# Kernel optimization log

Hardware: AMD Instinct MI355X
Metric: run time of the kernel (lower is better)

The kernel has to match this reference:

```python
import jax, jax.numpy as jnp
import numpy as np

B, E, I, H, O = 8192, 8, 512, 1024, 512


def setup_inputs() -> dict:
    key = jax.random.key(0)
    ks = jax.random.split(key, 8)
    # Xavier-uniform-ish scales for expert weights
    s1 = float(np.sqrt(6.0 / (I + H)))
    s2 = float(np.sqrt(6.0 / (H + H)))
    s3 = float(np.sqrt(6.0 / (H + O)))
    return {
        "X": jax.random.normal(ks[0], (B, I), dtype=jnp.float32),
        "W": jax.random.uniform(ks[1], (B, E), dtype=jnp.float32),
        "W1": jax.random.uniform(ks[2], (E, H, I), minval=-s1, maxval=s1, dtype=jnp.float32),
        "b1": jnp.zeros((E, H), dtype=jnp.float32),
        "W2": jax.random.uniform(ks[3], (E, H, H), minval=-s2, maxval=s2, dtype=jnp.float32),
        "b2": jnp.zeros((E, H), dtype=jnp.float32),
        "W3": jax.random.uniform(ks[4], (E, O, H), minval=-s3, maxval=s3, dtype=jnp.float32),
        "b3": jnp.zeros((E, O), dtype=jnp.float32),
    }


def reference(X, W, W1, b1, W2, b2, W3, b3):
    # NOTE: original torch code calls F.softmax(W, dim=1) but discards the
    # result; raw W is used as the per-expert mixing weight. We match that.
    # Layer 1: per-expert linear [B,E,H], then gate-weighted sum over E.
    pre1 = jnp.einsum('bi,ehi->beh', X, W1) + b1          # [B,E,H]
    mid1 = jax.nn.elu(jnp.einsum('be,beh->bh', W, pre1))  # [B,H]
    pre2 = jnp.einsum('bh,egh->beg', mid1, W2) + b2       # [B,E,H]
    mid2 = jax.nn.elu(jnp.einsum('be,beh->bh', W, pre2))  # [B,H]
    pre3 = jnp.einsum('bh,eoh->beo', mid2, W3) + b3       # [B,E,O]
    out = jnp.einsum('be,beo->bo', W, pre3)               # [B,O]
    return out
```

## Files before the change

kernel.cpp:

```cpp
#include <hip/hip_runtime.h>
#include <hip/hip_bf16.h>
#include <cstdint>
#include <cstddef>

typedef __attribute__((ext_vector_type(8))) short bf16x8;
typedef __attribute__((ext_vector_type(8))) unsigned short u16x8;
typedef __attribute__((ext_vector_type(4))) float f32x4;
typedef unsigned short u16;

__device__ __forceinline__ u16 f2bf(float f) {
    unsigned int u = __float_as_uint(f);
    u += 0x7fffu + ((u >> 16) & 1u);
    return (u16)(u >> 16);
}
__device__ __forceinline__ float bf2f(u16 u) {
    return __uint_as_float(((unsigned int)u) << 16);
}

__device__ __forceinline__ void gload16(const void* g, void* l) {
    __builtin_amdgcn_global_load_lds((const __attribute__((address_space(1))) void*)g,
                                     (__attribute__((address_space(3))) void*)l,
                                     16, 0, 0);
}

__global__ void cvt_f32_bf16(const float* __restrict__ in, u16* __restrict__ out, int n4) {
    int i = blockIdx.x * blockDim.x + threadIdx.x;
    if (i < n4) {
        float4 v = ((const float4*)in)[i];
        ushort4 o;
        o.x = f2bf(v.x); o.y = f2bf(v.y); o.z = f2bf(v.z); o.w = f2bf(v.w);
        ((ushort4*)out)[i] = o;
    }
}

__global__ void make_atilde_f32(const float* __restrict__ A, const float* __restrict__ gate,
                                u16* __restrict__ out, int log2K) {
    const size_t idx = ((size_t)blockIdx.x * 256 + threadIdx.x) * 8;
    const int K = 1 << log2K;
    const size_t b = idx >> (log2K + 3);
    const int rem = (int)(idx - (b << (log2K + 3)));
    const int e = rem >> log2K;
    const int k = rem & (K - 1);
    const float g = gate[b * 8 + e];
    const float* src = A + b * (size_t)K + k;
    float4 v0 = ((const float4*)src)[0];
    float4 v1 = ((const float4*)src)[1];
    u16x8 r;
    r[0] = f2bf(g * v0.x); r[1] = f2bf(g * v0.y); r[2] = f2bf(g * v0.z); r[3] = f2bf(g * v0.w);
    r[4] = f2bf(g * v1.x); r[5] = f2bf(g * v1.y); r[6] = f2bf(g * v1.z); r[7] = f2bf(g * v1.w);
    *(u16x8*)(out + idx) = r;
}

__global__ void make_atilde_bf16(const u16* __restrict__ A, const float* __restrict__ gate,
                                 u16* __restrict__ out, int log2K) {
    const size_t idx = ((size_t)blockIdx.x * 256 + threadIdx.x) * 8;
    const int K = 1 << log2K;
    const size_t b = idx >> (log2K + 3);
    const int rem = (int)(idx - (b << (log2K + 3)));
    const int e = rem >> log2K;
    const int k = rem & (K - 1);
    const float g = gate[b * 8 + e];
    u16x8 a = *(const u16x8*)(A + b * (size_t)K + k);
    u16x8 r;
    #pragma unroll
    for (int j = 0; j < 8; ++j) r[j] = f2bf(g * bf2f(a[j]));
    *(u16x8*)(out + idx) = r;
}

__global__ __launch_bounds__(512, 2)
void moe_gemm_8p(const u16* __restrict__ At, const u16* __restrict__ Bw,
                 float* __restrict__ P,
                 int N, int K, int Ktot, int log2nk, int kts, int bxbits) {
    __shared__ char lds[2][65536];

    const int tid  = threadIdx.x;
    const int lane = tid & 63;
    const int wave = tid >> 6;
    const int wm   = wave >> 2;
    const int wn   = wave & 3;
    const int fr   = lane & 15;
    const int fg   = lane >> 4;
    const int swz  = (fr & 7) << 4;

    const int bid  = blockIdx.x;
    const int wgid = (bid & 7) * 32 + (bid >> 3);
    const int bx   = wgid & ((1 << bxbits) - 1);
    const int by   = (wgid >> bxbits) & 31;
    const int s    = wgid >> (bxbits + 5);
    const int m0   = by * 256;
    const int n0   = bx * 256;

    int rowA[2], rowB[2], ldso[2];
    #pragma unroll
    for (int it = 0; it < 2; ++it) {
        const int o  = (it * 8 + wave) * 1024 + lane * 16;
        const int r  = o >> 7;
        const int cb = (o & 127) ^ ((r & 7) << 4);
        rowA[it] = r * (Ktot * 2) + cb;
        rowB[it] = r * (K * 2) + cb;
        ldso[it] = o;
    }

    const char* Ab0 = (const char*)(At + (size_t)m0 * Ktot);
    const char* Ab1 = Ab0 + (size_t)128 * Ktot * 2;
    const char* Bb0 = (const char*)(Bw + (size_t)n0 * K);
    const char* Bb1 = Bb0 + (size_t)128 * K * 2;
    const size_t Best = (size_t)N * K * 2;
    const int nkm = (1 << log2nk) - 1;
    const int kt0 = s * kts;

#define STAGE_A(BUF, KTG) do { \
    const char* _a0 = Ab0 + (size_t)(KTG) * 128; \
    const char* _a1 = Ab1 + (size_t)(KTG) * 128; \
    char* _l = lds[BUF]; \
    gload16(_a0 + rowA[0], _l + ldso[0]); \
    gload16(_a0 + rowA[1], _l + ldso[1]); \
    gload16(_a1 + rowA[0], _l + 16384 + ldso[0]); \
    gload16(_a1 + rowA[1], _l + 16384 + ldso[1]); \
} while (0)

#define STAGE_B(BUF, KTG) do { \
    const int _kg = (KTG); \
    const size_t _bo = (size_t)(_kg >> log2nk) * Best + (size_t)(_kg & nkm) * 128; \
    char* _l = lds[BUF] + 32768; \
    gload16(Bb0 + _bo + rowB[0], _l + ldso[0]); \
    gload16(Bb0 + _bo + rowB[1], _l + ldso[1]); \
    gload16(Bb1 + _bo + rowB[0], _l + 16384 + ldso[0]); \
    gload16(Bb1 + _bo + rowB[1], _l + 16384 + ldso[1]); \
} while (0)

#define PH_BAR() do { \
    __builtin_amdgcn_sched_barrier(0); \
    __builtin_amdgcn_s_barrier(); \
    __builtin_amdgcn_sched_barrier(0); \
} while (0)

    f32x4 acc[8][4];
    #pragma unroll
    for (int i = 0; i < 8; ++i)
        #pragma unroll
        for (int j = 0; j < 4; ++j) acc[i][j] = f32x4{0.f, 0.f, 0.f, 0.f};

    bf16x8 af[2][4], bfA[2][2], bfB[2][2];

    STAGE_A(0, kt0);
    STAGE_B(0, kt0);
    STAGE_A(1, kt0 + 1);
    __builtin_amdgcn_sched_barrier(0);
    asm volatile("s_waitcnt vmcnt(4)" ::: "memory");
    __builtin_amdgcn_s_barrier();
    __builtin_amdgcn_sched_barrier(0);

#define FRAME(BUF, TREL) do { \
    const int _tr = (TREL); \
    const char* _abase = lds[BUF] + wm * 16384 + fr * 128; \
    const char* _bbase = lds[BUF] + 32768 + (wn >> 1) * 16384 + ((wn & 1) * 64 + fr) * 128; \
    const int _k0 = (fg * 16) ^ swz; \
    const int _k1 = (64 + fg * 16) ^ swz; \
     \
    _Pragma("unroll") for (int i = 0; i < 4; ++i) { \
        af[0][i] = *(const bf16x8*)(_abase + i * 2048 + _k0); \
        af[1][i] = *(const bf16x8*)(_abase + i * 2048 + _k1); } \
    _Pragma("unroll") for (int j = 0; j < 2; ++j) { \
        bfA[0][j] = *(const bf16x8*)(_bbase + j * 2048 + _k0); \
        bfA[1][j] = *(const bf16x8*)(_bbase + j * 2048 + _k1); } \
    if (_tr + 1 < kts) STAGE_B((BUF) ^ 1, kt0 + _tr + 1); \
    PH_BAR(); \
    __builtin_amdgcn_s_setprio(1); \
    _Pragma("unroll") for (int i = 0; i < 4; ++i) \
    _Pragma("unroll") for (int j = 0; j < 2; ++j) { \
        acc[i][j] = __builtin_amdgcn_mfma_f32_16x16x32_bf16(af[0][i], bfA[0][j], acc[i][j], 0, 0, 0); \
        acc[i][j] = __builtin_amdgcn_mfma_f32_16x16x32_bf16(af[1][i], bfA[1][j], acc[i][j], 0, 0, 0); } \
    __builtin_amdgcn_s_setprio(0); \
    PH_BAR(); \
     \
    _Pragma("unroll") for (int j = 0; j < 2; ++j) { \
        bfB[0][j] = *(const bf16x8*)(_bbase + (2 + j) * 2048 + _k0); \
        bfB[1][j] = *(const bf16x8*)(_bbase + (2 + j) * 2048 + _k1); } \
    PH_BAR(); \
    __builtin_amdgcn_s_setprio(1); \
    _Pragma("unroll") for (int i = 0; i < 4; ++i) \
    _Pragma("unroll") for (int j = 0; j < 2; ++j) { \
        acc[i][2 + j] = __builtin_amdgcn_mfma_f32_16x16x32_bf16(af[0][i], bfB[0][j], acc[i][2 + j], 0, 0, 0); \
        acc[i][2 + j] = __builtin_amdgcn_mfma_f32_16x16x32_bf16(af[1][i], bfB[1][j], acc[i][2 + j], 0, 0, 0); } \
    __builtin_amdgcn_s_setprio(0); \
    PH_BAR(); \
     \
    _Pragma("unroll") for (int i = 0; i < 4; ++i) { \
        af[0][i] = *(const bf16x8*)(_abase + (4 + i) * 2048 + _k0); \
        af[1][i] = *(const bf16x8*)(_abase + (4 + i) * 2048 + _k1); } \
    PH_BAR(); \
    __builtin_amdgcn_s_setprio(1); \
    _Pragma("unroll") for (int i = 0; i < 4; ++i) \
    _Pragma("unroll") for (int j = 0; j < 2; ++j) { \
        acc[4 + i][2 + j] = __builtin_amdgcn_mfma_f32_16x16x32_bf16(af[0][i], bfB[0][j], acc[4 + i][2 + j], 0, 0, 0); \
        acc[4 + i][2 + j] = __builtin_amdgcn_mfma_f32_16x16x32_bf16(af[1][i], bfB[1][j], acc[4 + i][2 + j], 0, 0, 0); } \
    __builtin_amdgcn_s_setprio(0); \
    PH_BAR(); \
     \
    if (_tr + 2 < kts) { \
        STAGE_A(BUF, kt0 + _tr + 2); \
        __builtin_amdgcn_sched_barrier(0); \
        asm volatile("s_waitcnt vmcnt(4)" ::: "memory"); \
    } else { \
        __builtin_amdgcn_sched_barrier(0); \
        asm volatile("s_waitcnt vmcnt(0)" ::: "memory"); \
    } \
    __builtin_amdgcn_s_barrier(); \
    __builtin_amdgcn_sched_barrier(0); \
    __builtin_amdgcn_s_setprio(1); \
    _Pragma("unroll") for (int i = 0; i < 4; ++i) \
    _Pragma("unroll") for (int j = 0; j < 2; ++j) { \
        acc[4 + i][j] = __builtin_amdgcn_mfma_f32_16x16x32_bf16(af[0][i], bfA[0][j], acc[4 + i][j], 0, 0, 0); \
        acc[4 + i][j] = __builtin_amdgcn_mfma_f32_16x16x32_bf16(af[1][i], bfA[1][j], acc[4 + i][j], 0, 0, 0); } \
    __builtin_amdgcn_s_setprio(0); \
    PH_BAR(); \
} while (0)

    for (int t = 0; t < kts; t += 2) {
        FRAME(0, t);
        FRAME(1, t + 1);
    }

    float* Pb = P + ((size_t)s * 8192 + m0 + wm * 128) * N + (n0 + wn * 64);
    #pragma unroll
    for (int mi = 0; mi < 8; ++mi)
        #pragma unroll
        for (int j = 0; j < 4; ++j) {
            const int r = mi * 16 + fg * 4 + j;
            #pragma unroll
            for (int ni = 0; ni < 4; ++ni)
                Pb[(size_t)r * N + ni * 16 + fr] = acc[mi][ni][j];
        }
#undef FRAME
#undef PH_BAR
#undef STAGE_A
#undef STAGE_B
}

template<int S, bool ELU_ACT, bool OUT_BF16>
__global__ void moe_reduce(const float* __restrict__ P,
                           const float* __restrict__ gate,
                           const float* __restrict__ bias,
                           void* __restrict__ outp,
                           int log2N, int n4total) {
    const int stride = gridDim.x * blockDim.x;
    const size_t MN = ((size_t)n4total) * 4;
    for (int i = blockIdx.x * blockDim.x + threadIdx.x; i < n4total; i += stride) {
        const size_t el = (size_t)i * 4;
        const size_t b = el >> log2N;
        const int n = (int)(el & ((1 << log2N) - 1));
        float4 v = ((const float4*)P)[i];
        #pragma unroll
        for (int s = 1; s < S; ++s) {
            float4 p = *(const float4*)(P + (size_t)s * MN + el);
            v.x += p.x; v.y += p.y; v.z += p.z; v.w += p.w;
        }
        #pragma unroll
        for (int e = 0; e < 8; ++e) {
            const float g = gate[b * 8 + e];
            float4 bb = *(const float4*)(bias + ((size_t)e << log2N) + n);
            v.x += g * bb.x; v.y += g * bb.y; v.z += g * bb.z; v.w += g * bb.w;
        }
        if (ELU_ACT) {
            v.x = v.x > 0.f ? v.x : expm1f(v.x);
            v.y = v.y > 0.f ? v.y : expm1f(v.y);
            v.z = v.z > 0.f ? v.z : expm1f(v.z);
            v.w = v.w > 0.f ? v.w : expm1f(v.w);
        }
        if (OUT_BF16) {
            ushort4 o; o.x = f2bf(v.x); o.y = f2bf(v.y); o.z = f2bf(v.z); o.w = f2bf(v.w);
            ((ushort4*)outp)[i] = o;
        } else {
            ((float4*)outp)[i] = v;
        }
    }
}

extern "C" void kernel_launch(void* const* d_in, const int* in_sizes, int n_in,
                              void* d_out, int out_size, void* d_ws, size_t ws_size,
                              hipStream_t stream) {
    const float* X  = (const float*)d_in[0];
    const float* W  = (const float*)d_in[1];
    const float* W1 = (const float*)d_in[2];
    const float* b1 = (const float*)d_in[3];
    const float* W2 = (const float*)d_in[4];
    const float* b2 = (const float*)d_in[5];
    const float* W3 = (const float*)d_in[6];
    const float* b3 = (const float*)d_in[7];
    float* out = (float*)d_out;

    char* ws = (char*)d_ws;
    u16* W1b  = (u16*)ws;  ws += (size_t)8 * 1024 * 512 * 2;
    u16* W2b  = (u16*)ws;  ws += (size_t)8 * 1024 * 1024 * 2;
    u16* W3b  = (u16*)ws;  ws += (size_t)8 * 512 * 1024 * 2;
    u16* mid1 = (u16*)ws;  ws += (size_t)8192 * 1024 * 2;
    u16* mid2 = (u16*)ws;  ws += (size_t)8192 * 1024 * 2;
    u16* At1  = (u16*)ws;  ws += (size_t)8192 * 4096 * 2;
    u16* At2  = (u16*)ws;  ws += (size_t)8192 * 8192 * 2;

    float* P1 = (float*)At2;
    float* P2 = (float*)At1;
    float* P3 = (float*)At1;

    cvt_f32_bf16<<<4096, 256, 0, stream>>>(W1, W1b, 4194304 / 4);
    cvt_f32_bf16<<<8192, 256, 0, stream>>>(W2, W2b, 8388608 / 4);
    cvt_f32_bf16<<<4096, 256, 0, stream>>>(W3, W3b, 4194304 / 4);

    dim3 blk(256);

    make_atilde_f32<<<16384, blk, 0, stream>>>(X, W, At1, 9);
    moe_gemm_8p<<<256, 512, 0, stream>>>(At1, W1b, P1, 1024, 512, 4096, 3, 32, 2);
    moe_reduce<2, true, true><<<2048, blk, 0, stream>>>(P1, W, b1, (void*)mid1, 10, 8192 * 1024 / 4);

    make_atilde_bf16<<<32768, blk, 0, stream>>>(mid1, W, At2, 10);
    moe_gemm_8p<<<256, 512, 0, stream>>>(At2, W2b, P2, 1024, 1024, 8192, 4, 64, 2);
    moe_reduce<2, true, true><<<2048, blk, 0, stream>>>(P2, W, b2, (void*)mid2, 10, 8192 * 1024 / 4);

    make_atilde_bf16<<<32768, blk, 0, stream>>>(mid2, W, At2, 10);
    moe_gemm_8p<<<256, 512, 0, stream>>>(At2, W3b, P3, 512, 1024, 8192, 4, 32, 1);
    moe_reduce<4, false, false><<<2048, blk, 0, stream>>>(P3, W, b3, (void*)out, 9, 8192 * 512 / 4);
}
```

Measured before the change: 402.1 us.

## Cut GEMM K-loop barriers to two per tile and fuse reduce with gate-scaling

The GEMM main loop goes from eight workgroup barriers per K tile to two. The B stage for the next tile is issued up front, and the A restage is placed between the last two MFMA groups. Separately, the layer-2 split-K reduce, bias, ELU and the gate-scaled bf16 A-tilde construction are fused into one kernel, removing the mid2 round trip and one launch. With fewer barriers, waves drift further apart and lose the phase interleaving the old scheme enforced.

```diff
diff --git a/kernel.cpp b/kernel.cpp
--- a/kernel.cpp
+++ b/kernel.cpp
@@ -68,7 +68,7 @@
 }
 
 __global__ __launch_bounds__(512, 2)
-void moe_gemm_8p(const u16* __restrict__ At, const u16* __restrict__ Bw,
+void moe_gemm_2b(const u16* __restrict__ At, const u16* __restrict__ Bw,
                  float* __restrict__ P,
                  int N, int K, int Ktot, int log2nk, int kts, int bxbits) {
     __shared__ char lds[2][65536];
@@ -129,12 +129,6 @@
     gload16(Bb1 + _bo + rowB[1], _l + 16384 + ldso[1]); \
 } while (0)
 
-#define PH_BAR() do { \
-    __builtin_amdgcn_sched_barrier(0); \
-    __builtin_amdgcn_s_barrier(); \
-    __builtin_amdgcn_sched_barrier(0); \
-} while (0)
-
     f32x4 acc[8][4];
     #pragma unroll
     for (int i = 0; i < 8; ++i)
@@ -151,75 +145,89 @@
     __builtin_amdgcn_s_barrier();
     __builtin_amdgcn_sched_barrier(0);
 
-#define FRAME(BUF, TREL) do { \
-    const int _tr = (TREL); \
-    const char* _abase = lds[BUF] + wm * 16384 + fr * 128; \
-    const char* _bbase = lds[BUF] + 32768 + (wn >> 1) * 16384 + ((wn & 1) * 64 + fr) * 128; \
-    const int _k0 = (fg * 16) ^ swz; \
-    const int _k1 = (64 + fg * 16) ^ swz; \
-     \
-    _Pragma("unroll") for (int i = 0; i < 4; ++i) { \
-        af[0][i] = *(const bf16x8*)(_abase + i * 2048 + _k0); \
-        af[1][i] = *(const bf16x8*)(_abase + i * 2048 + _k1); } \
-    _Pragma("unroll") for (int j = 0; j < 2; ++j) { \
-        bfA[0][j] = *(const bf16x8*)(_bbase + j * 2048 + _k0); \
-        bfA[1][j] = *(const bf16x8*)(_bbase + j * 2048 + _k1); } \
-    if (_tr + 1 < kts) STAGE_B((BUF) ^ 1, kt0 + _tr + 1); \
-    PH_BAR(); \
-    __builtin_amdgcn_s_setprio(1); \
-    _Pragma("unroll") for (int i = 0; i < 4; ++i) \
-    _Pragma("unroll") for (int j = 0; j < 2; ++j) { \
-        acc[i][j] = __builtin_amdgcn_mfma_f32_16x16x32_bf16(af[0][i], bfA[0][j], acc[i][j], 0, 0, 0); \
-        acc[i][j] = __builtin_amdgcn_mfma_f32_16x16x32_bf16(af[1][i], bfA[1][j], acc[i][j], 0, 0, 0); } \
-    __builtin_amdgcn_s_setprio(0); \
-    PH_BAR(); \
-     \
-    _Pragma("unroll") for (int j = 0; j < 2; ++j) { \
-        bfB[0][j] = *(const bf16x8*)(_bbase + (2 + j) * 2048 + _k0); \
-        bfB[1][j] = *(const bf16x8*)(_bbase + (2 + j) * 2048 + _k1); } \
-    PH_BAR(); \
-    __builtin_amdgcn_s_setprio(1); \
-    _Pragma("unroll") for (int i = 0; i < 4; ++i) \
-    _Pragma("unroll") for (int j = 0; j < 2; ++j) { \
-        acc[i][2 + j] = __builtin_amdgcn_mfma_f32_16x16x32_bf16(af[0][i], bfB[0][j], acc[i][2 + j], 0, 0, 0); \
-        acc[i][2 + j] = __builtin_amdgcn_mfma_f32_16x16x32_bf16(af[1][i], bfB[1][j], acc[i][2 + j], 0, 0, 0); } \
-    __builtin_amdgcn_s_setprio(0); \
-    PH_BAR(); \
-     \
-    _Pragma("unroll") for (int i = 0; i < 4; ++i) { \
-        af[0][i] = *(const bf16x8*)(_abase + (4 + i) * 2048 + _k0); \
-        af[1][i] = *(const bf16x8*)(_abase + (4 + i) * 2048 + _k1); } \
-    PH_BAR(); \
-    __builtin_amdgcn_s_setprio(1); \
-    _Pragma("unroll") for (int i = 0; i < 4; ++i) \
-    _Pragma("unroll") for (int j = 0; j < 2; ++j) { \
-        acc[4 + i][2 + j] = __builtin_amdgcn_mfma_f32_16x16x32_bf16(af[0][i], bfB[0][j], acc[4 + i][2 + j], 0, 0, 0); \
-        acc[4 + i][2 + j] = __builtin_amdgcn_mfma_f32_16x16x32_bf16(af[1][i], bfB[1][j], acc[4 + i][2 + j], 0, 0, 0); } \
-    __builtin_amdgcn_s_setprio(0); \
-    PH_BAR(); \
-     \
-    if (_tr + 2 < kts) { \
-        STAGE_A(BUF, kt0 + _tr + 2); \
-        __builtin_amdgcn_sched_barrier(0); \
-        asm volatile("s_waitcnt vmcnt(4)" ::: "memory"); \
-    } else { \
-        __builtin_amdgcn_sched_barrier(0); \
-        asm volatile("s_waitcnt vmcnt(0)" ::: "memory"); \
-    } \
-    __builtin_amdgcn_s_barrier(); \
-    __builtin_amdgcn_sched_barrier(0); \
-    __builtin_amdgcn_s_setprio(1); \
-    _Pragma("unroll") for (int i = 0; i < 4; ++i) \
-    _Pragma("unroll") for (int j = 0; j < 2; ++j) { \
-        acc[4 + i][j] = __builtin_amdgcn_mfma_f32_16x16x32_bf16(af[0][i], bfA[0][j], acc[4 + i][j], 0, 0, 0); \
-        acc[4 + i][j] = __builtin_amdgcn_mfma_f32_16x16x32_bf16(af[1][i], bfA[1][j], acc[4 + i][j], 0, 0, 0); } \
-    __builtin_amdgcn_s_setprio(0); \
-    PH_BAR(); \
-} while (0)
-
-    for (int t = 0; t < kts; t += 2) {
-        FRAME(0, t);
-        FRAME(1, t + 1);
+    for (int t = 0; t < kts; ++t) {
+        const int BUF = t & 1;
+        const char* _abase = lds[BUF] + wm * 16384 + fr * 128;
+        const char* _bbase = lds[BUF] + 32768 + (wn >> 1) * 16384 + ((wn & 1) * 64 + fr) * 128;
+        const int k0 = (fg * 16) ^ swz;
+        const int k1 = (64 + fg * 16) ^ swz;
+
+        if (t + 1 < kts) STAGE_B(BUF ^ 1, kt0 + t + 1);
+
+        #pragma unroll
+        for (int i = 0; i < 4; ++i) {
+            af[0][i] = *(const bf16x8*)(_abase + i * 2048 + k0);
+            af[1][i] = *(const bf16x8*)(_abase + i * 2048 + k1);
+        }
+        #pragma unroll
+        for (int j = 0; j < 2; ++j) {
+            bfA[0][j] = *(const bf16x8*)(_bbase + j * 2048 + k0);
+            bfA[1][j] = *(const bf16x8*)(_bbase + j * 2048 + k1);
+        }
+        __builtin_amdgcn_s_setprio(1);
+        #pragma unroll
+        for (int i = 0; i < 4; ++i)
+            #pragma unroll
+            for (int j = 0; j < 2; ++j) {
+                acc[i][j] = __builtin_amdgcn_mfma_f32_16x16x32_bf16(af[0][i], bfA[0][j], acc[i][j], 0, 0, 0);
+                acc[i][j] = __builtin_amdgcn_mfma_f32_16x16x32_bf16(af[1][i], bfA[1][j], acc[i][j], 0, 0, 0);
+            }
+        __builtin_amdgcn_s_setprio(0);
+
+        #pragma unroll
+        for (int j = 0; j < 2; ++j) {
+            bfB[0][j] = *(const bf16x8*)(_bbase + (2 + j) * 2048 + k0);
+            bfB[1][j] = *(const bf16x8*)(_bbase + (2 + j) * 2048 + k1);
+        }
+        __builtin_amdgcn_s_setprio(1);
+        #pragma unroll
+        for (int i = 0; i < 4; ++i)
+            #pragma unroll
+            for (int j = 0; j < 2; ++j) {
+                acc[i][2 + j] = __builtin_amdgcn_mfma_f32_16x16x32_bf16(af[0][i], bfB[0][j], acc[i][2 + j], 0, 0, 0);
+                acc[i][2 + j] = __builtin_amdgcn_mfma_f32_16x16x32_bf16(af[1][i], bfB[1][j], acc[i][2 + j], 0, 0, 0);
+            }
+        __builtin_amdgcn_s_setprio(0);
+
+        #pragma unroll
+        for (int i = 0; i < 4; ++i) {
+            af[0][i] = *(const bf16x8*)(_abase + (4 + i) * 2048 + k0);
+            af[1][i] = *(const bf16x8*)(_abase + (4 + i) * 2048 + k1);
+        }
+        __builtin_amdgcn_s_setprio(1);
+        #pragma unroll
+        for (int i = 0; i < 4; ++i)
+            #pragma unroll
+            for (int j = 0; j < 2; ++j) {
+                acc[4 + i][2 + j] = __builtin_amdgcn_mfma_f32_16x16x32_bf16(af[0][i], bfB[0][j], acc[4 + i][2 + j], 0, 0, 0);
+                acc[4 + i][2 + j] = __builtin_amdgcn_mfma_f32_16x16x32_bf16(af[1][i], bfB[1][j], acc[4 + i][2 + j], 0, 0, 0);
+            }
+        __builtin_amdgcn_s_setprio(0);
+
+        __builtin_amdgcn_sched_barrier(0);
+        __builtin_amdgcn_s_barrier();
+        __builtin_amdgcn_sched_barrier(0);
+
+        if (t + 2 < kts) STAGE_A(BUF, kt0 + t + 2);
+
+        __builtin_amdgcn_s_setprio(1);
+        #pragma unroll
+        for (int i = 0; i < 4; ++i)
+            #pragma unroll
+            for (int j = 0; j < 2; ++j) {
+                acc[4 + i][j] = __builtin_amdgcn_mfma_f32_16x16x32_bf16(af[0][i], bfA[0][j], acc[4 + i][j], 0, 0, 0);
+                acc[4 + i][j] = __builtin_amdgcn_mfma_f32_16x16x32_bf16(af[1][i], bfA[1][j], acc[4 + i][j], 0, 0, 0);
+            }
+        __builtin_amdgcn_s_setprio(0);
+
+        __builtin_amdgcn_sched_barrier(0);
+        if (t + 2 < kts) {
+            asm volatile("s_waitcnt vmcnt(4)" ::: "memory");
+        } else {
+            asm volatile("s_waitcnt vmcnt(0)" ::: "memory");
+        }
+        __builtin_amdgcn_s_barrier();
+        __builtin_amdgcn_sched_barrier(0);
     }
 
     float* Pb = P + ((size_t)s * 8192 + m0 + wm * 128) * N + (n0 + wn * 64);
@@ -232,8 +240,6 @@
             for (int ni = 0; ni < 4; ++ni)
                 Pb[(size_t)r * N + ni * 16 + fr] = acc[mi][ni][j];
         }
-#undef FRAME
-#undef PH_BAR
 #undef STAGE_A
 #undef STAGE_B
 }
@@ -277,6 +283,46 @@
     }
 }
 
+__global__ void reduce_atilde2(const float* __restrict__ P,
+                               const float* __restrict__ gate,
+                               const float* __restrict__ bias,
+                               u16* __restrict__ At) {
+    const int idx = blockIdx.x * 256 + threadIdx.x;
+    const int h = (idx & 127) * 8;
+    const size_t b = idx >> 7;
+    const size_t MH = (size_t)8192 * 1024;
+    const float* p = P + b * 1024 + h;
+    float4 v0 = ((const float4*)p)[0];
+    float4 v1 = ((const float4*)p)[1];
+    {
+        const float* p1 = p + MH;
+        float4 a0 = ((const float4*)p1)[0], a1 = ((const float4*)p1)[1];
+        v0.x += a0.x; v0.y += a0.y; v0.z += a0.z; v0.w += a0.w;
+        v1.x += a1.x; v1.y += a1.y; v1.z += a1.z; v1.w += a1.w;
+    }
+    float4 g0 = *(const float4*)&gate[b * 8];
+    float4 g1 = *(const float4*)&gate[b * 8 + 4];
+    float gg[8] = {g0.x, g0.y, g0.z, g0.w, g1.x, g1.y, g1.z, g1.w};
+    #pragma unroll
+    for (int e = 0; e < 8; ++e) {
+        const float* bb = bias + e * 1024 + h;
+        float4 b0 = ((const float4*)bb)[0], b1 = ((const float4*)bb)[1];
+        v0.x += gg[e] * b0.x; v0.y += gg[e] * b0.y; v0.z += gg[e] * b0.z; v0.w += gg[e] * b0.w;
+        v1.x += gg[e] * b1.x; v1.y += gg[e] * b1.y; v1.z += gg[e] * b1.z; v1.w += gg[e] * b1.w;
+    }
+    float m[8] = {v0.x, v0.y, v0.z, v0.w, v1.x, v1.y, v1.z, v1.w};
+    #pragma unroll
+    for (int j = 0; j < 8; ++j) m[j] = m[j] > 0.f ? m[j] : expm1f(m[j]);
+    u16* o = At + b * 8192 + h;
+    #pragma unroll
+    for (int e = 0; e < 8; ++e) {
+        u16x8 r;
+        #pragma unroll
+        for (int j = 0; j < 8; ++j) r[j] = f2bf(gg[e] * m[j]);
+        *(u16x8*)(o + e * 1024) = r;
+    }
+}
+
 extern "C" void kernel_launch(void* const* d_in, const int* in_sizes, int n_in,
                               void* d_out, int out_size, void* d_ws, size_t ws_size,
                               hipStream_t stream) {
@@ -298,6 +344,7 @@
     u16* mid2 = (u16*)ws;  ws += (size_t)8192 * 1024 * 2;
     u16* At1  = (u16*)ws;  ws += (size_t)8192 * 4096 * 2;
     u16* At2  = (u16*)ws;  ws += (size_t)8192 * 8192 * 2;
+    (void)mid2;
 
     float* P1 = (float*)At2;
     float* P2 = (float*)At1;
@@ -310,14 +357,13 @@
     dim3 blk(256);
 
     make_atilde_f32<<<16384, blk, 0, stream>>>(X, W, At1, 9);
-    moe_gemm_8p<<<256, 512, 0, stream>>>(At1, W1b, P1, 1024, 512, 4096, 3, 32, 2);
+    moe_gemm_2b<<<256, 512, 0, stream>>>(At1, W1b, P1, 1024, 512, 4096, 3, 32, 2);
     moe_reduce<2, true, true><<<2048, blk, 0, stream>>>(P1, W, b1, (void*)mid1, 10, 8192 * 1024 / 4);
 
     make_atilde_bf16<<<32768, blk, 0, stream>>>(mid1, W, At2, 10);
-    moe_gemm_8p<<<256, 512, 0, stream>>>(At2, W2b, P2, 1024, 1024, 8192, 4, 64, 2);
-    moe_reduce<2, true, true><<<2048, blk, 0, stream>>>(P2, W, b2, (void*)mid2, 10, 8192 * 1024 / 4);
-
-    make_atilde_bf16<<<32768, blk, 0, stream>>>(mid2, W, At2, 10);
-    moe_gemm_8p<<<256, 512, 0, stream>>>(At2, W3b, P3, 512, 1024, 8192, 4, 32, 1);
+    moe_gemm_2b<<<256, 512, 0, stream>>>(At2, W2b, P2, 1024, 1024, 8192, 4, 64, 2);
+    reduce_atilde2<<<4096, blk, 0, stream>>>(P2, W, b2, At2);
+
+    moe_gemm_2b<<<256, 512, 0, stream>>>(At2, W3b, P3, 512, 1024, 8192, 4, 32, 1);
     moe_reduce<4, false, false><<<2048, blk, 0, stream>>>(P3, W, b3, (void*)out, 9, 8192 * 512 / 4);
 }
```

Result: faster. 378.4 us (-5.9%).

## Restructure GEMM pipeline to one barrier per k-tile and fuse reduce with atilde

Applied to the files above, without the earlier changes.

The GEMM main loop drops the phased schedule, which had many barriers per tile and an A-tile prefetch two stages ahead. It now issues the next A and B tiles into the other buffer at the start of each k-tile and synchronizes once at the end with a full vmcnt(0) wait. Separately, the layer-2 split-K reduction, bias, ELU and gate-scaled bf16 A-tilde construction are fused into one kernel, removing the mid2 round trip and a launch. The simpler pipeline reduces barrier overhead but exposes global-load latency more, since it waits for all loads at every tile.

```diff
diff --git a/kernel.cpp b/kernel.cpp
--- a/kernel.cpp
+++ b/kernel.cpp
@@ -68,7 +68,7 @@
 }
 
 __global__ __launch_bounds__(512, 2)
-void moe_gemm_8p(const u16* __restrict__ At, const u16* __restrict__ Bw,
+void moe_gemm_1b(const u16* __restrict__ At, const u16* __restrict__ Bw,
                  float* __restrict__ P,
                  int N, int K, int Ktot, int log2nk, int kts, int bxbits) {
     __shared__ char lds[2][65536];
@@ -129,97 +129,77 @@
     gload16(Bb1 + _bo + rowB[1], _l + 16384 + ldso[1]); \
 } while (0)
 
-#define PH_BAR() do { \
+    f32x4 acc[8][4];
+    #pragma unroll
+    for (int i = 0; i < 8; ++i)
+        #pragma unroll
+        for (int j = 0; j < 4; ++j) acc[i][j] = f32x4{0.f, 0.f, 0.f, 0.f};
+
+    bf16x8 af[2][4], bfA[2][2], bfB[2][2];
+
+    const char* aB[2], * bB[2];
+    #pragma unroll
+    for (int u = 0; u < 2; ++u) {
+        aB[u] = lds[u] + wm * 16384 + fr * 128;
+        bB[u] = lds[u] + 32768 + (wn >> 1) * 16384 + ((wn & 1) * 64 + fr) * 128;
+    }
+    const int k0 = (fg * 16) ^ swz;
+    const int k1 = (64 + fg * 16) ^ swz;
+
+    STAGE_A(0, kt0);
+    STAGE_B(0, kt0);
+    __builtin_amdgcn_sched_barrier(0);
+    asm volatile("s_waitcnt vmcnt(0)" ::: "memory");
+    __builtin_amdgcn_s_barrier();
+    __builtin_amdgcn_sched_barrier(0);
+
+#define KTILE(BUF, T) do { \
+    const int _t = (T); \
+    if (_t + 1 < kts) STAGE_B((BUF) ^ 1, kt0 + _t + 1); \
+    _Pragma("unroll") for (int i = 0; i < 4; ++i) { \
+        af[0][i] = *(const bf16x8*)(aB[BUF] + i * 2048 + k0); \
+        af[1][i] = *(const bf16x8*)(aB[BUF] + i * 2048 + k1); } \
+    _Pragma("unroll") for (int j = 0; j < 2; ++j) { \
+        bfA[0][j] = *(const bf16x8*)(bB[BUF] + j * 2048 + k0); \
+        bfA[1][j] = *(const bf16x8*)(bB[BUF] + j * 2048 + k1); } \
+    if (_t + 1 < kts) STAGE_A((BUF) ^ 1, kt0 + _t + 1); \
+    __builtin_amdgcn_s_setprio(1); \
+    _Pragma("unroll") for (int i = 0; i < 4; ++i) \
+    _Pragma("unroll") for (int j = 0; j < 2; ++j) { \
+        acc[i][j] = __builtin_amdgcn_mfma_f32_16x16x32_bf16(af[0][i], bfA[0][j], acc[i][j], 0, 0, 0); \
+        acc[i][j] = __builtin_amdgcn_mfma_f32_16x16x32_bf16(af[1][i], bfA[1][j], acc[i][j], 0, 0, 0); } \
+    __builtin_amdgcn_s_setprio(0); \
+    _Pragma("unroll") for (int j = 0; j < 2; ++j) { \
+        bfB[0][j] = *(const bf16x8*)(bB[BUF] + (2 + j) * 2048 + k0); \
+        bfB[1][j] = *(const bf16x8*)(bB[BUF] + (2 + j) * 2048 + k1); } \
+    __builtin_amdgcn_s_setprio(1); \
+    _Pragma("unroll") for (int i = 0; i < 4; ++i) \
+    _Pragma("unroll") for (int j = 0; j < 2; ++j) { \
+        acc[i][2 + j] = __builtin_amdgcn_mfma_f32_16x16x32_bf16(af[0][i], bfB[0][j], acc[i][2 + j], 0, 0, 0); \
+        acc[i][2 + j] = __builtin_amdgcn_mfma_f32_16x16x32_bf16(af[1][i], bfB[1][j], acc[i][2 + j], 0, 0, 0); } \
+    __builtin_amdgcn_s_setprio(0); \
+    _Pragma("unroll") for (int i = 0; i < 4; ++i) { \
+        af[0][i] = *(const bf16x8*)(aB[BUF] + (4 + i) * 2048 + k0); \
+        af[1][i] = *(const bf16x8*)(aB[BUF] + (4 + i) * 2048 + k1); } \
+    __builtin_amdgcn_s_setprio(1); \
+    _Pragma("unroll") for (int i = 0; i < 4; ++i) \
+    _Pragma("unroll") for (int j = 0; j < 2; ++j) { \
+        acc[4 + i][2 + j] = __builtin_amdgcn_mfma_f32_16x16x32_bf16(af[0][i], bfB[0][j], acc[4 + i][2 + j], 0, 0, 0); \
+        acc[4 + i][2 + j] = __builtin_amdgcn_mfma_f32_16x16x32_bf16(af[1][i], bfB[1][j], acc[4 + i][2 + j], 0, 0, 0); } \
+    _Pragma("unroll") for (int i = 0; i < 4; ++i) \
+    _Pragma("unroll") for (int j = 0; j < 2; ++j) { \
+        acc[4 + i][j] = __builtin_amdgcn_mfma_f32_16x16x32_bf16(af[0][i], bfA[0][j], acc[4 + i][j], 0, 0, 0); \
+        acc[4 + i][j] = __builtin_amdgcn_mfma_f32_16x16x32_bf16(af[1][i], bfA[1][j], acc[4 + i][j], 0, 0, 0); } \
+    __builtin_amdgcn_s_setprio(0); \
     __builtin_amdgcn_sched_barrier(0); \
+    asm volatile("s_waitcnt vmcnt(0)" ::: "memory"); \
     __builtin_amdgcn_s_barrier(); \
     __builtin_amdgcn_sched_barrier(0); \
 } while (0)
 
-    f32x4 acc[8][4];
-    #pragma unroll
-    for (int i = 0; i < 8; ++i)
-        #pragma unroll
-        for (int j = 0; j < 4; ++j) acc[i][j] = f32x4{0.f, 0.f, 0.f, 0.f};
-
-    bf16x8 af[2][4], bfA[2][2], bfB[2][2];
-
-    STAGE_A(0, kt0);
-    STAGE_B(0, kt0);
-    STAGE_A(1, kt0 + 1);
-    __builtin_amdgcn_sched_barrier(0);
-    asm volatile("s_waitcnt vmcnt(4)" ::: "memory");
-    __builtin_amdgcn_s_barrier();
-    __builtin_amdgcn_sched_barrier(0);
-
-#define FRAME(BUF, TREL) do { \
-    const int _tr = (TREL); \
-    const char* _abase = lds[BUF] + wm * 16384 + fr * 128; \
-    const char* _bbase = lds[BUF] + 32768 + (wn >> 1) * 16384 + ((wn & 1) * 64 + fr) * 128; \
-    const int _k0 = (fg * 16) ^ swz; \
-    const int _k1 = (64 + fg * 16) ^ swz; \
-     \
-    _Pragma("unroll") for (int i = 0; i < 4; ++i) { \
-        af[0][i] = *(const bf16x8*)(_abase + i * 2048 + _k0); \
-        af[1][i] = *(const bf16x8*)(_abase + i * 2048 + _k1); } \
-    _Pragma("unroll") for (int j = 0; j < 2; ++j) { \
-        bfA[0][j] = *(const bf16x8*)(_bbase + j * 2048 + _k0); \
-        bfA[1][j] = *(const bf16x8*)(_bbase + j * 2048 + _k1); } \
-    if (_tr + 1 < kts) STAGE_B((BUF) ^ 1, kt0 + _tr + 1); \
-    PH_BAR(); \
-    __builtin_amdgcn_s_setprio(1); \
-    _Pragma("unroll") for (int i = 0; i < 4; ++i) \
-    _Pragma("unroll") for (int j = 0; j < 2; ++j) { \
-        acc[i][j] = __builtin_amdgcn_mfma_f32_16x16x32_bf16(af[0][i], bfA[0][j], acc[i][j], 0, 0, 0); \
-        acc[i][j] = __builtin_amdgcn_mfma_f32_16x16x32_bf16(af[1][i], bfA[1][j], acc[i][j], 0, 0, 0); } \
-    __builtin_amdgcn_s_setprio(0); \
-    PH_BAR(); \
-     \
-    _Pragma("unroll") for (int j = 0; j < 2; ++j) { \
-        bfB[0][j] = *(const bf16x8*)(_bbase + (2 + j) * 2048 + _k0); \
-        bfB[1][j] = *(const bf16x8*)(_bbase + (2 + j) * 2048 + _k1); } \
-    PH_BAR(); \
-    __builtin_amdgcn_s_setprio(1); \
-    _Pragma("unroll") for (int i = 0; i < 4; ++i) \
-    _Pragma("unroll") for (int j = 0; j < 2; ++j) { \
-        acc[i][2 + j] = __builtin_amdgcn_mfma_f32_16x16x32_bf16(af[0][i], bfB[0][j], acc[i][2 + j], 0, 0, 0); \
-        acc[i][2 + j] = __builtin_amdgcn_mfma_f32_16x16x32_bf16(af[1][i], bfB[1][j], acc[i][2 + j], 0, 0, 0); } \
-    __builtin_amdgcn_s_setprio(0); \
-    PH_BAR(); \
-     \
-    _Pragma("unroll") for (int i = 0; i < 4; ++i) { \
-        af[0][i] = *(const bf16x8*)(_abase + (4 + i) * 2048 + _k0); \
-        af[1][i] = *(const bf16x8*)(_abase + (4 + i) * 2048 + _k1); } \
-    PH_BAR(); \
-    __builtin_amdgcn_s_setprio(1); \
-    _Pragma("unroll") for (int i = 0; i < 4; ++i) \
-    _Pragma("unroll") for (int j = 0; j < 2; ++j) { \
-        acc[4 + i][2 + j] = __builtin_amdgcn_mfma_f32_16x16x32_bf16(af[0][i], bfB[0][j], acc[4 + i][2 + j], 0, 0, 0); \
-        acc[4 + i][2 + j] = __builtin_amdgcn_mfma_f32_16x16x32_bf16(af[1][i], bfB[1][j], acc[4 + i][2 + j], 0, 0, 0); } \
-    __builtin_amdgcn_s_setprio(0); \
-    PH_BAR(); \
-     \
-    if (_tr + 2 < kts) { \
-        STAGE_A(BUF, kt0 + _tr + 2); \
-        __builtin_amdgcn_sched_barrier(0); \
-        asm volatile("s_waitcnt vmcnt(4)" ::: "memory"); \
-    } else { \
-        __builtin_amdgcn_sched_barrier(0); \
-        asm volatile("s_waitcnt vmcnt(0)" ::: "memory"); \
-    } \
-    __builtin_amdgcn_s_barrier(); \
-    __builtin_amdgcn_sched_barrier(0); \
-    __builtin_amdgcn_s_setprio(1); \
-    _Pragma("unroll") for (int i = 0; i < 4; ++i) \
-    _Pragma("unroll") for (int j = 0; j < 2; ++j) { \
-        acc[4 + i][j] = __builtin_amdgcn_mfma_f32_16x16x32_bf16(af[0][i], bfA[0][j], acc[4 + i][j], 0, 0, 0); \
-        acc[4 + i][j] = __builtin_amdgcn_mfma_f32_16x16x32_bf16(af[1][i], bfA[1][j], acc[4 + i][j], 0, 0, 0); } \
-    __builtin_amdgcn_s_setprio(0); \
-    PH_BAR(); \
-} while (0)
-
     for (int t = 0; t < kts; t += 2) {
-        FRAME(0, t);
-        FRAME(1, t + 1);
+        KTILE(0, t);
+        KTILE(1, t + 1);
     }
 
     float* Pb = P + ((size_t)s * 8192 + m0 + wm * 128) * N + (n0 + wn * 64);
@@ -232,8 +212,7 @@
             for (int ni = 0; ni < 4; ++ni)
                 Pb[(size_t)r * N + ni * 16 + fr] = acc[mi][ni][j];
         }
-#undef FRAME
-#undef PH_BAR
+#undef KTILE
 #undef STAGE_A
 #undef STAGE_B
 }
@@ -277,6 +256,46 @@
     }
 }
 
+__global__ void reduce_atilde2(const float* __restrict__ P,
+                               const float* __restrict__ gate,
+                               const float* __restrict__ bias,
+                               u16* __restrict__ At) {
+    const int idx = blockIdx.x * 256 + threadIdx.x;
+    const int h = (idx & 127) * 8;
+    const size_t b = idx >> 7;
+    const size_t MH = (size_t)8192 * 1024;
+    const float* p = P + b * 1024 + h;
+    float4 v0 = ((const float4*)p)[0];
+    float4 v1 = ((const float4*)p)[1];
+    {
+        const float* p1 = p + MH;
+        float4 a0 = ((const float4*)p1)[0], a1 = ((const float4*)p1)[1];
+        v0.x += a0.x; v0.y += a0.y; v0.z += a0.z; v0.w += a0.w;
+        v1.x += a1.x; v1.y += a1.y; v1.z += a1.z; v1.w += a1.w;
+    }
+    float4 g0 = *(const float4*)&gate[b * 8];
+    float4 g1 = *(const float4*)&gate[b * 8 + 4];
+    float gg[8] = {g0.x, g0.y, g0.z, g0.w, g1.x, g1.y, g1.z, g1.w};
+    #pragma unroll
+    for (int e = 0; e < 8; ++e) {
+        const float* bb = bias + e * 1024 + h;
+        float4 b0 = ((const float4*)bb)[0], b1 = ((const float4*)bb)[1];
+        v0.x += gg[e] * b0.x; v0.y += gg[e] * b0.y; v0.z += gg[e] * b0.z; v0.w += gg[e] * b0.w;
+        v1.x += gg[e] * b1.x; v1.y += gg[e] * b1.y; v1.z += gg[e] * b1.z; v1.w += gg[e] * b1.w;
+    }
+    float m[8] = {v0.x, v0.y, v0.z, v0.w, v1.x, v1.y, v1.z, v1.w};
+    #pragma unroll
+    for (int j = 0; j < 8; ++j) m[j] = m[j] > 0.f ? m[j] : expm1f(m[j]);
+    u16* o = At + b * 8192 + h;
+    #pragma unroll
+    for (int e = 0; e < 8; ++e) {
+        u16x8 r;
+        #pragma unroll
+        for (int j = 0; j < 8; ++j) r[j] = f2bf(gg[e] * m[j]);
+        *(u16x8*)(o + e * 1024) = r;
+    }
+}
+
 extern "C" void kernel_launch(void* const* d_in, const int* in_sizes, int n_in,
                               void* d_out, int out_size, void* d_ws, size_t ws_size,
                               hipStream_t stream) {
@@ -298,6 +317,7 @@
     u16* mid2 = (u16*)ws;  ws += (size_t)8192 * 1024 * 2;
     u16* At1  = (u16*)ws;  ws += (size_t)8192 * 4096 * 2;
     u16* At2  = (u16*)ws;  ws += (size_t)8192 * 8192 * 2;
+    (void)mid2;
 
     float* P1 = (float*)At2;
     float* P2 = (float*)At1;
@@ -310,14 +330,13 @@
     dim3 blk(256);
 
     make_atilde_f32<<<16384, blk, 0, stream>>>(X, W, At1, 9);
-    moe_gemm_8p<<<256, 512, 0, stream>>>(At1, W1b, P1, 1024, 512, 4096, 3, 32, 2);
+    moe_gemm_1b<<<256, 512, 0, stream>>>(At1, W1b, P1, 1024, 512, 4096, 3, 32, 2);
     moe_reduce<2, true, true><<<2048, blk, 0, stream>>>(P1, W, b1, (void*)mid1, 10, 8192 * 1024 / 4);
 
     make_atilde_bf16<<<32768, blk, 0, stream>>>(mid1, W, At2, 10);
-    moe_gemm_8p<<<256, 512, 0, stream>>>(At2, W2b, P2, 1024, 1024, 8192, 4, 64, 2);
-    moe_reduce<2, true, true><<<2048, blk, 0, stream>>>(P2, W, b2, (void*)mid2, 10, 8192 * 1024 / 4);
-
-    make_atilde_bf16<<<32768, blk, 0, stream>>>(mid2, W, At2, 10);
-    moe_gemm_8p<<<256, 512, 0, stream>>>(At2, W3b, P3, 512, 1024, 8192, 4, 32, 1);
+    moe_gemm_1b<<<256, 512, 0, stream>>>(At2, W2b, P2, 1024, 1024, 8192, 4, 64, 2);
+    reduce_atilde2<<<4096, blk, 0, stream>>>(P2, W, b2, At2);
+
+    moe_gemm_1b<<<256, 512, 0, stream>>>(At2, W3b, P3, 512, 1024, 8192, 4, 32, 1);
     moe_reduce<4, false, false><<<2048, blk, 0, stream>>>(P3, W, b3, (void*)out, 9, 8192 * 512 / 4);
 }
```

Result: faster. 374.9 us (-6.8%).
